# Kernel tuning notes

Measured on AMD Instinct MI355X. Metric: run time of the kernel, lower is better.

## Reference

```python
import jax, jax.numpy as jnp
import numpy as np

BS, S, D, H, KVH, HD = 2, 2048, 2048, 32, 8, 64
N_REP = H // KVH
N_DOCS = 4


def setup_inputs() -> dict:
    key = jax.random.key(0)
    ks = jax.random.split(key, 7)
    x = jax.random.normal(ks[0], (BS, S, D), dtype=jnp.float32)
    # RoPE table (llama theta=10000), stored as real (cos, sin) pairs: [S, HD//2, 2]
    inv_freq = 1.0 / (10000.0 ** (jnp.arange(0, HD, 2, dtype=jnp.float32) / HD))
    ang = jnp.arange(S, dtype=jnp.float32)[:, None] * inv_freq[None, :]  # [S, HD//2]
    freqs_cis = jnp.stack([jnp.cos(ang), jnp.sin(ang)], axis=-1)
    # packed-document ids, non-decreasing along sequence: [BS, S]
    sequence_id = jnp.sort(
        jax.random.randint(ks[1], (BS, S), 0, N_DOCS, dtype=jnp.int32), axis=-1
    )
    std = 0.02
    wq = jax.random.normal(ks[2], (H * HD, D), dtype=jnp.float32) * std
    wk = jax.random.normal(ks[3], (KVH * HD, D), dtype=jnp.float32) * std
    wv = jax.random.normal(ks[4], (KVH * HD, D), dtype=jnp.float32) * std
    wo = jax.random.normal(ks[5], (D, H * HD), dtype=jnp.float32) * std
    return {"x": x, "freqs_cis": freqs_cis, "sequence_id": sequence_id,
            "wq": wq, "wk": wk, "wv": wv, "wo": wo}


def _apply_rope(t, freqs_cis):
    # t: [b, s, h, hd]; freqs_cis: [s, hd//2, 2] (cos, sin)
    b, s, h, hd = t.shape
    tp = t.reshape(b, s, h, hd // 2, 2)
    t0, t1 = tp[..., 0], tp[..., 1]
    cos = freqs_cis[None, :, None, :, 0]
    sin = freqs_cis[None, :, None, :, 1]
    o0 = t0 * cos - t1 * sin
    o1 = t0 * sin + t1 * cos
    return jnp.stack([o0, o1], axis=-1).reshape(b, s, h, hd)


def reference(x, freqs_cis, sequence_id, wq, wk, wv, wo):
    bs, s, _ = x.shape
    xq = (x @ wq.T).reshape(bs, s, H, HD)
    xk = (x @ wk.T).reshape(bs, s, KVH, HD)
    xv = (x @ wv.T).reshape(bs, s, KVH, HD)
    xq = _apply_rope(xq, freqs_cis)
    xk = _apply_rope(xk, freqs_cis)
    # GQA without materializing repeated KV: group queries by kv head
    q = xq.reshape(bs, s, KVH, N_REP, HD).transpose(0, 2, 3, 1, 4)  # [b,g,r,s,d]
    k = xk.transpose(0, 2, 1, 3)  # [b,g,s,d]
    v = xv.transpose(0, 2, 1, 3)  # [b,g,s,d]
    scale = 1.0 / jnp.sqrt(jnp.float32(HD))
    scores = jnp.einsum("bgrqd,bgkd->bgrqk", q, k) * scale
    # document-causal mask: same sequence_id AND causal
    causal = jnp.tril(jnp.ones((s, s), dtype=bool))
    same_doc = sequence_id[:, :, None] == sequence_id[:, None, :]  # [b,s,s]
    mask = (causal[None] & same_doc)[:, None, None, :, :]  # [b,1,1,s,s]
    scores = jnp.where(mask, scores, jnp.float32(-1e30))
    probs = jax.nn.softmax(scores, axis=-1)
    out = jnp.einsum("bgrqk,bgkd->bgrqd", probs, v)  # [b,g,r,s,d]
    out = out.transpose(0, 3, 1, 2, 4).reshape(bs, s, H * HD)
    return out @ wo.T
```

## Files before the change

kernel.cpp:

```cpp
#include <hip/hip_runtime.h>
#include <hip/hip_bf16.h>

typedef __attribute__((ext_vector_type(8))) short bf16x8;
typedef __attribute__((ext_vector_type(4))) float f32x4;

#define MFMA16(A, B, C) __builtin_amdgcn_mfma_f32_16x16x32_bf16(A, B, C, 0, 0, 0)

__device__ __forceinline__ unsigned short f2bf(float f) {
    unsigned int u = __float_as_uint(f);
    u += 0x7fffu + ((u >> 16) & 1u);
    return (unsigned short)(u >> 16);
}
__device__ __forceinline__ float bf2f(unsigned short h) {
    return __uint_as_float(((unsigned int)h) << 16);
}
__device__ __forceinline__ unsigned int pack_bf2(float lo, float hi) {
    __hip_bfloat162 h = __float22bfloat162_rn(make_float2(lo, hi));
    return *reinterpret_cast<unsigned int*>(&h);
}

__device__ __forceinline__ void gload_lds16(const void* g, void* l) {
    __builtin_amdgcn_global_load_lds(
        (__attribute__((address_space(1))) unsigned int*)g,
        (__attribute__((address_space(3))) unsigned int*)l, 16, 0, 0);
}

__device__ __forceinline__ int swz128(int by) {
    return by ^ (((by >> 7) & 7) << 4);
}

__global__ void cvt_kernel(const float* __restrict__ in, unsigned short* __restrict__ out, int n4) {
    const int i = blockIdx.x * 256 + threadIdx.x;
    if (i >= n4) return;
    const float4 v = ((const float4*)in)[i];
    uint2 o;
    o.x = pack_bf2(v.x, v.y);
    o.y = pack_bf2(v.z, v.w);
    ((uint2*)out)[i] = o;
}

__global__ void docstart_kernel(const int* __restrict__ sid, int* __restrict__ ds) {
    const int i = blockIdx.x * 256 + threadIdx.x;
    const int b = i >> 11, s = i & 2047;
    const int* row = sid + b * 2048;
    const int v = row[s];
    int lo = 0, hi = s;
    while (lo < hi) { const int mid = (lo + hi) >> 1; if (row[mid] < v) lo = mid + 1; else hi = mid; }
    ds[i] = lo;
}

#define QKV_K 2048
#define QKV_NT 32
__global__ __launch_bounds__(512, 2) void gemm_qkv8(
    const unsigned short* __restrict__ A,
    const unsigned short* __restrict__ B,
    unsigned short* __restrict__ oq,
    unsigned short* __restrict__ ok,
    unsigned short* __restrict__ ov)
{
    __shared__ __align__(16) unsigned short S[2][2][2][8192];
    const int tid = threadIdx.x, lane = tid & 63, w = tid >> 6;
    const int wr = w >> 2, wc = w & 3;
    const int lr = lane & 15, lc = lane >> 4;

    int bid = blockIdx.x;
    bid = (bid & 7) * 24 + (bid >> 3);
    const int m0 = (bid / 12) * 256, n0 = (bid % 12) * 256;

    const int o0 = (w << 11) + (lane << 4);
    const int o1 = o0 + 1024;
    const int v0 = swz128(o0);
    const int v1 = swz128(o1);
    const int r0 = v0 >> 7, c0 = (v0 & 127) >> 1;
    const int r1 = v1 >> 7, c1 = (v1 & 127) >> 1;
    const size_t aoff0 = (size_t)(m0 + r0) * QKV_K + c0;
    const size_t aoff1 = (size_t)(m0 + r1) * QKV_K + c1;
    const size_t boff0 = (size_t)(n0 + r0) * QKV_K + c0;
    const size_t boff1 = (size_t)(n0 + r1) * QKV_K + c1;
    const int d0 = o0 >> 1, d1 = o1 >> 1;

    f32x4 acc[2][2][4][2];
#pragma unroll
    for (int a = 0; a < 2; a++)
#pragma unroll
        for (int bq = 0; bq < 2; bq++)
#pragma unroll
            for (int i = 0; i < 4; i++)
#pragma unroll
                for (int j = 0; j < 2; j++) acc[a][bq][i][j] = (f32x4){0.f, 0.f, 0.f, 0.f};

    bf16x8 Af[4][2], Bf0[2][2], Bf1[2][2];

    auto STAGE_A = [&](int bf, int h, int kt) {
        gload_lds16(A + aoff0 + (size_t)h * 128 * QKV_K + (size_t)kt * 64, &S[bf][0][h][d0]);
        gload_lds16(A + aoff1 + (size_t)h * 128 * QKV_K + (size_t)kt * 64, &S[bf][0][h][d1]);
    };
    auto STAGE_B = [&](int bf, int h, int kt) {
        gload_lds16(B + boff0 + (size_t)h * 128 * QKV_K + (size_t)kt * 64, &S[bf][1][h][d0]);
        gload_lds16(B + boff1 + (size_t)h * 128 * QKV_K + (size_t)kt * 64, &S[bf][1][h][d1]);
    };
    auto LDA = [&](int bf, int mh) {
#pragma unroll
        for (int i = 0; i < 4; i++)
#pragma unroll
            for (int kh = 0; kh < 2; kh++) {
                const int by = swz128(((wr * 64 + i * 16 + lr) << 7) + (kh << 6) + (lc << 4));
                Af[i][kh] = *(const bf16x8*)((const char*)&S[bf][0][mh][0] + by);
            }
    };
    auto LDB = [&](int bf, int nh, bf16x8 (&Bf)[2][2]) {
#pragma unroll
        for (int j = 0; j < 2; j++)
#pragma unroll
            for (int kh = 0; kh < 2; kh++) {
                const int by = swz128(((wc * 32 + j * 16 + lr) << 7) + (kh << 6) + (lc << 4));
                Bf[j][kh] = *(const bf16x8*)((const char*)&S[bf][1][nh][0] + by);
            }
    };
    auto QUAD = [&](f32x4 (&ac)[4][2], bf16x8 (&Bf)[2][2]) {
        __builtin_amdgcn_s_setprio(1);
#pragma unroll
        for (int i = 0; i < 4; i++)
#pragma unroll
            for (int j = 0; j < 2; j++)
#pragma unroll
                for (int kh = 0; kh < 2; kh++)
                    ac[i][j] = MFMA16(Af[i][kh], Bf[j][kh], ac[i][j]);
        __builtin_amdgcn_s_setprio(0);
    };

#define BAR() __builtin_amdgcn_s_barrier()
#define LGKM0() asm volatile("s_waitcnt lgkmcnt(0)" ::: "memory")

    STAGE_A(0, 0, 0); STAGE_A(0, 1, 0); STAGE_B(0, 0, 0); STAGE_B(0, 1, 0);
    STAGE_A(1, 0, 1); STAGE_B(1, 1, 1); STAGE_A(1, 1, 1);
    asm volatile("s_waitcnt vmcnt(6)" ::: "memory");
    BAR();

    auto GROUP = [&](int g, int bf) {
        LDA(bf, 0); LDB(bf, 0, Bf0);
        if (g + 1 < QKV_NT) STAGE_B(bf ^ 1, 0, g + 1);
        BAR(); LGKM0();
        QUAD(acc[0][0], Bf0);
        BAR();
        LDB(bf, 1, Bf1);
        if (g + 2 < QKV_NT) STAGE_A(bf, 0, g + 2);
        BAR(); LGKM0();
        QUAD(acc[0][1], Bf1);
        BAR();
        LDA(bf, 1);
        if (g + 2 < QKV_NT) STAGE_B(bf, 1, g + 2);
        BAR(); LGKM0();
        QUAD(acc[1][1], Bf1);
        BAR();
        if (g + 2 < QKV_NT) STAGE_A(bf, 1, g + 2);
        BAR();
        QUAD(acc[1][0], Bf0);
        if (g == QKV_NT - 2) { asm volatile("s_waitcnt vmcnt(0)" ::: "memory"); }
        else                 { asm volatile("s_waitcnt vmcnt(6)" ::: "memory"); }
        BAR();
    };

#pragma unroll 1
    for (int g = 0; g < QKV_NT; g += 2) {
        GROUP(g, 0);
        GROUP(g + 1, 1);
    }

#pragma unroll
    for (int mh = 0; mh < 2; mh++)
#pragma unroll
        for (int nh = 0; nh < 2; nh++)
#pragma unroll
            for (int i = 0; i < 4; i++)
#pragma unroll
                for (int j = 0; j < 2; j++) {
                    const int n = n0 + nh * 128 + wc * 32 + j * 16 + lr;
                    const int d = n & 63;
                    const int hh6 = n >> 6;
#pragma unroll
                    for (int r = 0; r < 4; r++) {
                        const int m = m0 + mh * 128 + wr * 64 + i * 16 + lc * 4 + r;
                        const int bb = m >> 11, s = m & 2047;
                        const unsigned short val = f2bf(acc[mh][nh][i][j][r]);
                        if (n < 2048) {
                            oq[((((size_t)bb * 32 + hh6) * 2048 + s) << 6) + d] = val;
                        } else if (n < 2560) {
                            ok[((((size_t)bb * 8 + (hh6 - 32)) * 2048 + s) << 6) + d] = val;
                        } else {
                            ov[((((size_t)bb * 8 + (hh6 - 40)) * 2048 + s) << 6) + d] = val;
                        }
                    }
                }
}
#undef BAR
#undef LGKM0

template <int EPI>
__global__ __launch_bounds__(256) void gemm_bt(
    const unsigned short* __restrict__ A,
    const unsigned short* __restrict__ B,
    int K, int N,
    unsigned short* __restrict__ oq,
    unsigned short* __restrict__ ok,
    unsigned short* __restrict__ ov,
    float* __restrict__ of)
{
    __shared__ __align__(16) unsigned short sA[128 * 32];
    __shared__ __align__(16) unsigned short sB[128 * 32];
    const int tid = threadIdx.x;
    const int lane = tid & 63, wave = tid >> 6;
    const int wr = wave >> 1, wc = wave & 1;
    const int lr = lane & 15, lc = lane >> 4;

    int bid = blockIdx.y * gridDim.x + blockIdx.x;
    const int cpx = (gridDim.x * gridDim.y) >> 3;
    bid = (bid & 7) * cpx + (bid >> 3);
    const int m0 = (bid / gridDim.x) * 128, n0 = (bid % gridDim.x) * 128;

    f32x4 acc[4][4];
#pragma unroll
    for (int i = 0; i < 4; i++)
#pragma unroll
        for (int j = 0; j < 4; j++) acc[i][j] = (f32x4){0.f, 0.f, 0.f, 0.f};

    const int u0 = tid, u1 = tid + 256;
    for (int k0 = 0; k0 < K; k0 += 32) {
        __syncthreads();
        gload_lds16(A + (size_t)(m0 + (u0 >> 2)) * K + k0 + (u0 & 3) * 8, &sA[u0 * 8]);
        gload_lds16(A + (size_t)(m0 + (u1 >> 2)) * K + k0 + (u1 & 3) * 8, &sA[u1 * 8]);
        gload_lds16(B + (size_t)(n0 + (u0 >> 2)) * K + k0 + (u0 & 3) * 8, &sB[u0 * 8]);
        gload_lds16(B + (size_t)(n0 + (u1 >> 2)) * K + k0 + (u1 & 3) * 8, &sB[u1 * 8]);
        __syncthreads();
        bf16x8 af[4], bfv[4];
#pragma unroll
        for (int i = 0; i < 4; i++) {
            af[i]  = *(const bf16x8*)&sA[(wr * 64 + i * 16 + lr) * 32 + lc * 8];
            bfv[i] = *(const bf16x8*)&sB[(wc * 64 + i * 16 + lr) * 32 + lc * 8];
        }
#pragma unroll
        for (int i = 0; i < 4; i++)
#pragma unroll
            for (int j = 0; j < 4; j++) acc[i][j] = MFMA16(af[i], bfv[j], acc[i][j]);
    }

    if (EPI == 0) {
#pragma unroll
        for (int i = 0; i < 4; i++) {
#pragma unroll
            for (int j = 0; j < 4; j++) {
                const int n = n0 + wc * 64 + j * 16 + lr;
                const int d = n & 63;
#pragma unroll
                for (int r = 0; r < 4; r++) {
                    const int m = m0 + wr * 64 + i * 16 + lc * 4 + r;
                    const int bb = m >> 11, s = m & 2047;
                    const unsigned short val = f2bf(acc[i][j][r]);
                    if (n < 2048) {
                        const int hh = n >> 6;
                        oq[((((size_t)bb * 32 + hh) * 2048 + s) << 6) + d] = val;
                    } else if (n < 2560) {
                        const int hh = (n >> 6) - 32;
                        ok[((((size_t)bb * 8 + hh) * 2048 + s) << 6) + d] = val;
                    } else {
                        const int hh = (n >> 6) - 40;
                        ov[((((size_t)bb * 8 + hh) * 2048 + s) << 6) + d] = val;
                    }
                }
            }
        }
    } else {
#pragma unroll
        for (int i = 0; i < 4; i++)
#pragma unroll
            for (int j = 0; j < 4; j++)
#pragma unroll
                for (int r = 0; r < 4; r++) {
                    const int m = m0 + wr * 64 + i * 16 + lc * 4 + r;
                    const int n = n0 + wc * 64 + j * 16 + lr;
                    of[(size_t)m * N + n] = acc[i][j][r];
                }
    }
}

__global__ void rope_kernel(unsigned short* __restrict__ Qb,
                            unsigned short* __restrict__ Kb,
                            const float* __restrict__ fc)
{
    const int NQ = 2 * 32 * 2048 * 32;
    int i = blockIdx.x * 256 + threadIdx.x;
    unsigned short* base;
    if (i < NQ) base = Qb;
    else { base = Kb; i -= NQ; }
    const int p = i & 31, s = (i >> 5) & 2047, bh = i >> 16;
    const size_t off = (((size_t)bh * 2048 + s) << 6) + p * 2;
    const unsigned int w = *(const unsigned int*)&base[off];
    const float t0 = bf2f((unsigned short)(w & 0xffffu));
    const float t1 = bf2f((unsigned short)(w >> 16));
    const float c = fc[(s * 32 + p) * 2], sn = fc[(s * 32 + p) * 2 + 1];
    *(unsigned int*)&base[off] = pack_bf2(t0 * c - t1 * sn, t0 * sn + t1 * c);
}

__global__ __launch_bounds__(256) void attn_kernel(
    const unsigned short* __restrict__ Q,
    const unsigned short* __restrict__ K,
    const unsigned short* __restrict__ V,
    const int* __restrict__ dstart,
    unsigned short* __restrict__ AO)
{
    const int qt = 31 - blockIdx.x;
    const int h = blockIdx.y, b = blockIdx.z;
    const int kvh = h >> 2;
    const int tid = threadIdx.x, lane = tid & 63, wave = tid >> 6;
    const int lr = lane & 15, lc = lane >> 4;
    const int q0 = qt * 64;
    const int qw = q0 + wave * 16;

    __shared__ __align__(16) unsigned short sK[64 * 64];
    __shared__ __align__(16) unsigned short sVt[64][72];

    const unsigned short* Qh = Q + (((size_t)b * 32 + h) * 2048) * 64;
    const unsigned short* Kh = K + (((size_t)b * 8 + kvh) * 2048) * 64;
    const unsigned short* Vh = V + (((size_t)b * 8 + kvh) * 2048) * 64;

    const bf16x8 qf0 = *(const bf16x8*)&Qh[(size_t)(qw + lr) * 64 + lc * 8];
    const bf16x8 qf1 = *(const bf16x8*)&Qh[(size_t)(qw + lr) * 64 + 32 + lc * 8];

    const int qglob = qw + lr;
    const int dsl = dstart[b * 2048 + qglob];
    const int ds_wmin = dstart[b * 2048 + qw];
    const int t0 = dstart[b * 2048 + q0] & ~63;

    float mrow = -1e30f, lrow = 0.f;
    f32x4 oacc[4];
#pragma unroll
    for (int j = 0; j < 4; j++) oacc[j] = (f32x4){0.f, 0.f, 0.f, 0.f};

    for (int t = t0; t < q0 + 64; t += 64) {
        __syncthreads();
        {
            int slot = tid;
            int r = slot >> 3, c = slot & 7;
            gload_lds16(Kh + (size_t)(t + r) * 64 + ((c ^ (r & 7)) * 8), &sK[slot * 8]);
            slot = tid + 256; r = slot >> 3; c = slot & 7;
            gload_lds16(Kh + (size_t)(t + r) * 64 + ((c ^ (r & 7)) * 8), &sK[slot * 8]);
        }
        {
            const int w8 = wave * 8;
            const uint4 va = *(const uint4*)&Vh[(size_t)(t + lane) * 64 + w8];
            const uint4 vb = *(const uint4*)&Vh[(size_t)(t + lane) * 64 + 32 + w8];
            const unsigned short* pa = (const unsigned short*)&va;
            const unsigned short* pb = (const unsigned short*)&vb;
#pragma unroll
            for (int e = 0; e < 8; e++) sVt[w8 + e][lane] = pa[e];
#pragma unroll
            for (int e = 0; e < 8; e++) sVt[32 + w8 + e][lane] = pb[e];
        }
        asm volatile("s_waitcnt vmcnt(0)" ::: "memory");
        __syncthreads();
        if (t > qw + 15 || t + 63 < ds_wmin) continue;

        f32x4 sc[4];
#pragma unroll
        for (int kk = 0; kk < 4; kk++) {
            const int krow = kk * 16 + lr;
            const bf16x8 kf0 = *(const bf16x8*)&sK[krow * 64 + ((lc ^ (lr & 7)) * 8)];
            const bf16x8 kf1 = *(const bf16x8*)&sK[krow * 64 + (((4 + lc) ^ (lr & 7)) * 8)];
            f32x4 a = (f32x4){0.f, 0.f, 0.f, 0.f};
            a = MFMA16(kf0, qf0, a);
            a = MFMA16(kf1, qf1, a);
            sc[kk] = a;
        }
        float vmax = -3e38f;
#pragma unroll
        for (int kk = 0; kk < 4; kk++)
#pragma unroll
            for (int r = 0; r < 4; r++) {
                const int kpos = t + kk * 16 + lc * 4 + r;
                const bool okm = (kpos <= qglob) && (kpos >= dsl);
                sc[kk][r] = okm ? sc[kk][r] * 0.125f : -3e38f;
                vmax = fmaxf(vmax, sc[kk][r]);
            }
        vmax = fmaxf(vmax, __shfl_xor(vmax, 16));
        vmax = fmaxf(vmax, __shfl_xor(vmax, 32));
        const float mnew = fmaxf(mrow, vmax);
        const float corr = __expf(mrow - mnew);
        mrow = mnew;

        float rsum = 0.f;
        unsigned int pk[4][2];
#pragma unroll
        for (int kk = 0; kk < 4; kk++) {
            const float p0 = __expf(sc[kk][0] - mnew);
            const float p1 = __expf(sc[kk][1] - mnew);
            const float p2 = __expf(sc[kk][2] - mnew);
            const float p3 = __expf(sc[kk][3] - mnew);
            rsum += (p0 + p1) + (p2 + p3);
            pk[kk][0] = pack_bf2(p0, p1);
            pk[kk][1] = pack_bf2(p2, p3);
        }
        rsum += __shfl_xor(rsum, 16);
        rsum += __shfl_xor(rsum, 32);
        lrow = lrow * corr + rsum;
#pragma unroll
        for (int j = 0; j < 4; j++)
#pragma unroll
            for (int r = 0; r < 4; r++) oacc[j][r] *= corr;

        const int srcEven = 32 * (lc & 1) + lr;
        const int srcOdd  = srcEven + 16;
        const bool hiKK = (lc & 2) != 0;
        union { unsigned int w[4]; bf16x8 v; } B0, B1;
        {
            unsigned int a, c;
            a = __shfl(pk[0][0], srcEven); c = __shfl(pk[1][0], srcEven); B0.w[0] = hiKK ? c : a;
            a = __shfl(pk[0][1], srcEven); c = __shfl(pk[1][1], srcEven); B0.w[1] = hiKK ? c : a;
            a = __shfl(pk[0][0], srcOdd);  c = __shfl(pk[1][0], srcOdd);  B0.w[2] = hiKK ? c : a;
            a = __shfl(pk[0][1], srcOdd);  c = __shfl(pk[1][1], srcOdd);  B0.w[3] = hiKK ? c : a;
            a = __shfl(pk[2][0], srcEven); c = __shfl(pk[3][0], srcEven); B1.w[0] = hiKK ? c : a;
            a = __shfl(pk[2][1], srcEven); c = __shfl(pk[3][1], srcEven); B1.w[1] = hiKK ? c : a;
            a = __shfl(pk[2][0], srcOdd);  c = __shfl(pk[3][0], srcOdd);  B1.w[2] = hiKK ? c : a;
            a = __shfl(pk[2][1], srcOdd);  c = __shfl(pk[3][1], srcOdd);  B1.w[3] = hiKK ? c : a;
        }

#pragma unroll
        for (int j = 0; j < 4; j++) {
            const bf16x8 a0 = *(const bf16x8*)&sVt[j * 16 + lr][lc * 8];
            const bf16x8 a1 = *(const bf16x8*)&sVt[j * 16 + lr][32 + lc * 8];
            oacc[j] = MFMA16(a0, B0.v, oacc[j]);
            oacc[j] = MFMA16(a1, B1.v, oacc[j]);
        }
    }

    __syncthreads();
    const float inv = 1.0f / lrow;
#pragma unroll
    for (int j = 0; j < 4; j++)
#pragma unroll
        for (int p = 0; p < 2; p++) {
            const unsigned int w = pack_bf2(oacc[j][2 * p] * inv, oacc[j][2 * p + 1] * inv);
            *(unsigned int*)&sVt[wave * 16 + lr][j * 16 + lc * 4 + 2 * p] = w;
        }
    __syncthreads();
#pragma unroll
    for (int half = 0; half < 2; half++) {
        const int c = lane + 64 * half;
        const int row = c >> 3, ch = c & 7;
        const uint4 o = *(const uint4*)&sVt[wave * 16 + row][ch * 8];
        *(uint4*)&AO[((size_t)b * 2048 + qw + row) * 2048 + h * 64 + ch * 8] = o;
    }
}

extern "C" void kernel_launch(void* const* d_in, const int* in_sizes, int n_in,
                              void* d_out, int out_size, void* d_ws, size_t ws_size,
                              hipStream_t stream) {
    const float* x  = (const float*)d_in[0];
    const float* fc = (const float*)d_in[1];
    const int* sid  = (const int*)d_in[2];
    const float* wq = (const float*)d_in[3];
    const float* wk = (const float*)d_in[4];
    const float* wv = (const float*)d_in[5];
    const float* wo = (const float*)d_in[6];
    float* out = (float*)d_out;

    unsigned short* xb   = (unsigned short*)d_ws;
    unsigned short* wqkv = xb + (size_t)4096 * 2048;
    unsigned short* wob  = wqkv + (size_t)3072 * 2048;
    unsigned short* Qb   = wob + (size_t)2048 * 2048;
    unsigned short* Kb   = Qb + (size_t)2 * 32 * 2048 * 64;
    unsigned short* Vb   = Kb + (size_t)2 * 8 * 2048 * 64;
    unsigned short* AO   = Vb + (size_t)2 * 8 * 2048 * 64;
    int* dstart = (int*)(AO + (size_t)4096 * 2048);

    cvt_kernel<<<8192, 256, 0, stream>>>(x, xb, 2097152);
    cvt_kernel<<<4096, 256, 0, stream>>>(wq, wqkv, 1048576);
    cvt_kernel<<<1024, 256, 0, stream>>>(wk, wqkv + (size_t)2048 * 2048, 262144);
    cvt_kernel<<<1024, 256, 0, stream>>>(wv, wqkv + (size_t)2560 * 2048, 262144);
    cvt_kernel<<<4096, 256, 0, stream>>>(wo, wob, 1048576);
    docstart_kernel<<<16, 256, 0, stream>>>(sid, dstart);
    gemm_qkv8<<<dim3(192), 512, 0, stream>>>(xb, wqkv, Qb, Kb, Vb);
    rope_kernel<<<20480, 256, 0, stream>>>(Qb, Kb, fc);
    attn_kernel<<<dim3(32, 32, 2), 256, 0, stream>>>(Qb, Kb, Vb, dstart, AO);
    gemm_bt<1><<<dim3(16, 32), 256, 0, stream>>>(AO, wob, 2048, 2048, nullptr, nullptr, nullptr, out);
}
```

Measured before the change: 209.4 us.

## Fuse RoPE into QKV GEMM epilogue, merge converts, double-buffer attention K/V

Five fp32-to-bf16 conversion launches become one kernel. RoPE moves into the QKV GEMM epilogue: each pair partner comes from a lane shuffle and cos/sin are read from the table, so the separate RoPE read-modify-write pass over Q and K goes away. The attention kernel double-buffers its K/V shared-memory tiles, prefetching the next tile while the current one is computed, at the cost of twice the LDS and possibly lower occupancy.

```diff
diff --git a/kernel.cpp b/kernel.cpp
--- a/kernel.cpp
+++ b/kernel.cpp
@@ -29,14 +29,26 @@
     return by ^ (((by >> 7) & 7) << 4);
 }
 
-__global__ void cvt_kernel(const float* __restrict__ in, unsigned short* __restrict__ out, int n4) {
+__global__ void cvt_all_kernel(const float* __restrict__ x,  const float* __restrict__ wq,
+                               const float* __restrict__ wk, const float* __restrict__ wv,
+                               const float* __restrict__ wo,
+                               unsigned short* __restrict__ xb,
+                               unsigned short* __restrict__ wqkv,
+                               unsigned short* __restrict__ wob) {
     const int i = blockIdx.x * 256 + threadIdx.x;
-    if (i >= n4) return;
-    const float4 v = ((const float4*)in)[i];
+    const float* src;
+    unsigned short* dst;
+    int off;
+    if (i < 2097152)      { src = x;  dst = xb;   off = i; }
+    else if (i < 3145728) { src = wq; dst = wqkv; off = i - 2097152; }
+    else if (i < 3407872) { src = wk; dst = wqkv + (size_t)2048 * 2048; off = i - 3145728; }
+    else if (i < 3670016) { src = wv; dst = wqkv + (size_t)2560 * 2048; off = i - 3407872; }
+    else                  { src = wo; dst = wob;  off = i - 3670016; }
+    const float4 v = ((const float4*)src)[off];
     uint2 o;
     o.x = pack_bf2(v.x, v.y);
     o.y = pack_bf2(v.z, v.w);
-    ((uint2*)out)[i] = o;
+    ((uint2*)dst)[off] = o;
 }
 
 __global__ void docstart_kernel(const int* __restrict__ sid, int* __restrict__ ds) {
@@ -54,6 +66,7 @@
 __global__ __launch_bounds__(512, 2) void gemm_qkv8(
     const unsigned short* __restrict__ A,
     const unsigned short* __restrict__ B,
+    const float* __restrict__ fc,
     unsigned short* __restrict__ oq,
     unsigned short* __restrict__ ok,
     unsigned short* __restrict__ ov)
@@ -69,8 +82,7 @@
 
     const int o0 = (w << 11) + (lane << 4);
     const int o1 = o0 + 1024;
-    const int v0 = swz128(o0);
-    const int v1 = swz128(o1);
+    const int v0 = swz128(o0), v1 = swz128(o1);
     const int r0 = v0 >> 7, c0 = (v0 & 127) >> 1;
     const int r1 = v1 >> 7, c1 = (v1 & 127) >> 1;
     const size_t aoff0 = (size_t)(m0 + r0) * QKV_K + c0;
@@ -177,12 +189,21 @@
                 for (int j = 0; j < 2; j++) {
                     const int n = n0 + nh * 128 + wc * 32 + j * 16 + lr;
                     const int d = n & 63;
+                    const int p = d >> 1;
                     const int hh6 = n >> 6;
+                    const bool isV = (n >= 2560);
 #pragma unroll
                     for (int r = 0; r < 4; r++) {
                         const int m = m0 + mh * 128 + wr * 64 + i * 16 + lc * 4 + r;
                         const int bb = m >> 11, s = m & 2047;
-                        const unsigned short val = f2bf(acc[mh][nh][i][j][r]);
+                        float v = acc[mh][nh][i][j][r];
+                        const float pv = __shfl_xor(v, 1);
+                        if (!isV) {
+                            const float2 cs = *(const float2*)&fc[((s << 5) + p) << 1];
+                            v = (d & 1) ? fmaf(v, cs.x, pv * cs.y)
+                                        : fmaf(v, cs.x, -pv * cs.y);
+                        }
+                        const unsigned short val = f2bf(v);
                         if (n < 2048) {
                             oq[((((size_t)bb * 32 + hh6) * 2048 + s) << 6) + d] = val;
                         } else if (n < 2560) {
@@ -283,24 +304,6 @@
     }
 }
 
-__global__ void rope_kernel(unsigned short* __restrict__ Qb,
-                            unsigned short* __restrict__ Kb,
-                            const float* __restrict__ fc)
-{
-    const int NQ = 2 * 32 * 2048 * 32;
-    int i = blockIdx.x * 256 + threadIdx.x;
-    unsigned short* base;
-    if (i < NQ) base = Qb;
-    else { base = Kb; i -= NQ; }
-    const int p = i & 31, s = (i >> 5) & 2047, bh = i >> 16;
-    const size_t off = (((size_t)bh * 2048 + s) << 6) + p * 2;
-    const unsigned int w = *(const unsigned int*)&base[off];
-    const float t0 = bf2f((unsigned short)(w & 0xffffu));
-    const float t1 = bf2f((unsigned short)(w >> 16));
-    const float c = fc[(s * 32 + p) * 2], sn = fc[(s * 32 + p) * 2 + 1];
-    *(unsigned int*)&base[off] = pack_bf2(t0 * c - t1 * sn, t0 * sn + t1 * c);
-}
-
 __global__ __launch_bounds__(256) void attn_kernel(
     const unsigned short* __restrict__ Q,
     const unsigned short* __restrict__ K,
@@ -316,8 +319,8 @@
     const int q0 = qt * 64;
     const int qw = q0 + wave * 16;
 
-    __shared__ __align__(16) unsigned short sK[64 * 64];
-    __shared__ __align__(16) unsigned short sVt[64][72];
+    __shared__ __align__(16) unsigned short sK[2][64 * 64];
+    __shared__ __align__(16) unsigned short sVt[2][64][72];
 
     const unsigned short* Qh = Q + (((size_t)b * 32 + h) * 2048) * 64;
     const unsigned short* Kh = K + (((size_t)b * 8 + kvh) * 2048) * 64;
@@ -331,87 +334,100 @@
     const int ds_wmin = dstart[b * 2048 + qw];
     const int t0 = dstart[b * 2048 + q0] & ~63;
 
+    const int w8 = wave * 8;
+    const int slot0 = tid,       kr0 = slot0 >> 3, kc0 = slot0 & 7;
+    const int slot1 = tid + 256, kr1 = slot1 >> 3, kc1 = slot1 & 7;
+
+    auto STAGE_K = [&](int t, int c) {
+        gload_lds16(Kh + (size_t)(t + kr0) * 64 + ((kc0 ^ (kr0 & 7)) * 8), &sK[c][slot0 * 8]);
+        gload_lds16(Kh + (size_t)(t + kr1) * 64 + ((kc1 ^ (kr1 & 7)) * 8), &sK[c][slot1 * 8]);
+    };
+    auto WRITE_V = [&](const uint4& va, const uint4& vb, int c) {
+        const unsigned short* pa = (const unsigned short*)&va;
+        const unsigned short* pb = (const unsigned short*)&vb;
+#pragma unroll
+        for (int e = 0; e < 8; e++) sVt[c][w8 + e][lane] = pa[e];
+#pragma unroll
+        for (int e = 0; e < 8; e++) sVt[c][32 + w8 + e][lane] = pb[e];
+    };
+
     float mrow = -1e30f, lrow = 0.f;
     f32x4 oacc[4];
 #pragma unroll
     for (int j = 0; j < 4; j++) oacc[j] = (f32x4){0.f, 0.f, 0.f, 0.f};
 
-    for (int t = t0; t < q0 + 64; t += 64) {
-        __syncthreads();
-        {
-            int slot = tid;
-            int r = slot >> 3, c = slot & 7;
-            gload_lds16(Kh + (size_t)(t + r) * 64 + ((c ^ (r & 7)) * 8), &sK[slot * 8]);
-            slot = tid + 256; r = slot >> 3; c = slot & 7;
-            gload_lds16(Kh + (size_t)(t + r) * 64 + ((c ^ (r & 7)) * 8), &sK[slot * 8]);
-        }
-        {
-            const int w8 = wave * 8;
-            const uint4 va = *(const uint4*)&Vh[(size_t)(t + lane) * 64 + w8];
-            const uint4 vb = *(const uint4*)&Vh[(size_t)(t + lane) * 64 + 32 + w8];
-            const unsigned short* pa = (const unsigned short*)&va;
-            const unsigned short* pb = (const unsigned short*)&vb;
-#pragma unroll
-            for (int e = 0; e < 8; e++) sVt[w8 + e][lane] = pa[e];
-#pragma unroll
-            for (int e = 0; e < 8; e++) sVt[32 + w8 + e][lane] = pb[e];
-        }
+    STAGE_K(t0, 0);
+    {
+        const uint4 va = *(const uint4*)&Vh[(size_t)(t0 + lane) * 64 + w8];
+        const uint4 vb = *(const uint4*)&Vh[(size_t)(t0 + lane) * 64 + 32 + w8];
         asm volatile("s_waitcnt vmcnt(0)" ::: "memory");
-        __syncthreads();
-        if (t > qw + 15 || t + 63 < ds_wmin) continue;
-
-        f32x4 sc[4];
-#pragma unroll
-        for (int kk = 0; kk < 4; kk++) {
-            const int krow = kk * 16 + lr;
-            const bf16x8 kf0 = *(const bf16x8*)&sK[krow * 64 + ((lc ^ (lr & 7)) * 8)];
-            const bf16x8 kf1 = *(const bf16x8*)&sK[krow * 64 + (((4 + lc) ^ (lr & 7)) * 8)];
-            f32x4 a = (f32x4){0.f, 0.f, 0.f, 0.f};
-            a = MFMA16(kf0, qf0, a);
-            a = MFMA16(kf1, qf1, a);
-            sc[kk] = a;
-        }
-        float vmax = -3e38f;
-#pragma unroll
-        for (int kk = 0; kk < 4; kk++)
-#pragma unroll
-            for (int r = 0; r < 4; r++) {
-                const int kpos = t + kk * 16 + lc * 4 + r;
-                const bool okm = (kpos <= qglob) && (kpos >= dsl);
-                sc[kk][r] = okm ? sc[kk][r] * 0.125f : -3e38f;
-                vmax = fmaxf(vmax, sc[kk][r]);
+        WRITE_V(va, vb, 0);
+    }
+    __syncthreads();
+
+    int cb = 0;
+    for (int t = t0; t < q0 + 64; t += 64, cb ^= 1) {
+        const bool more = (t < q0);
+        uint4 va, vb;
+        if (more) {
+            STAGE_K(t + 64, cb ^ 1);
+            va = *(const uint4*)&Vh[(size_t)(t + 64 + lane) * 64 + w8];
+            vb = *(const uint4*)&Vh[(size_t)(t + 64 + lane) * 64 + 32 + w8];
+        }
+        const bool act = !(t > qw + 15 || t + 63 < ds_wmin);
+        union { unsigned int w[4]; bf16x8 v; } B0, B1;
+
+        if (act) {
+            f32x4 sc[4];
+#pragma unroll
+            for (int kk = 0; kk < 4; kk++) {
+                const int krow = kk * 16 + lr;
+                const bf16x8 kf0 = *(const bf16x8*)&sK[cb][krow * 64 + ((lc ^ (lr & 7)) * 8)];
+                const bf16x8 kf1 = *(const bf16x8*)&sK[cb][krow * 64 + (((4 + lc) ^ (lr & 7)) * 8)];
+                f32x4 a = (f32x4){0.f, 0.f, 0.f, 0.f};
+                a = MFMA16(kf0, qf0, a);
+                a = MFMA16(kf1, qf1, a);
+                sc[kk] = a;
             }
-        vmax = fmaxf(vmax, __shfl_xor(vmax, 16));
-        vmax = fmaxf(vmax, __shfl_xor(vmax, 32));
-        const float mnew = fmaxf(mrow, vmax);
-        const float corr = __expf(mrow - mnew);
-        mrow = mnew;
-
-        float rsum = 0.f;
-        unsigned int pk[4][2];
-#pragma unroll
-        for (int kk = 0; kk < 4; kk++) {
-            const float p0 = __expf(sc[kk][0] - mnew);
-            const float p1 = __expf(sc[kk][1] - mnew);
-            const float p2 = __expf(sc[kk][2] - mnew);
-            const float p3 = __expf(sc[kk][3] - mnew);
-            rsum += (p0 + p1) + (p2 + p3);
-            pk[kk][0] = pack_bf2(p0, p1);
-            pk[kk][1] = pack_bf2(p2, p3);
-        }
-        rsum += __shfl_xor(rsum, 16);
-        rsum += __shfl_xor(rsum, 32);
-        lrow = lrow * corr + rsum;
-#pragma unroll
-        for (int j = 0; j < 4; j++)
-#pragma unroll
-            for (int r = 0; r < 4; r++) oacc[j][r] *= corr;
-
-        const int srcEven = 32 * (lc & 1) + lr;
-        const int srcOdd  = srcEven + 16;
-        const bool hiKK = (lc & 2) != 0;
-        union { unsigned int w[4]; bf16x8 v; } B0, B1;
-        {
+            float vmax = -3e38f;
+#pragma unroll
+            for (int kk = 0; kk < 4; kk++)
+#pragma unroll
+                for (int r = 0; r < 4; r++) {
+                    const int kpos = t + kk * 16 + lc * 4 + r;
+                    const bool okm = (kpos <= qglob) && (kpos >= dsl);
+                    sc[kk][r] = okm ? sc[kk][r] * 0.125f : -3e38f;
+                    vmax = fmaxf(vmax, sc[kk][r]);
+                }
+            vmax = fmaxf(vmax, __shfl_xor(vmax, 16));
+            vmax = fmaxf(vmax, __shfl_xor(vmax, 32));
+            const float mnew = fmaxf(mrow, vmax);
+            const float corr = __expf(mrow - mnew);
+            mrow = mnew;
+
+            float rsum = 0.f;
+            unsigned int pk[4][2];
+#pragma unroll
+            for (int kk = 0; kk < 4; kk++) {
+                const float p0 = __expf(sc[kk][0] - mnew);
+                const float p1 = __expf(sc[kk][1] - mnew);
+                const float p2 = __expf(sc[kk][2] - mnew);
+                const float p3 = __expf(sc[kk][3] - mnew);
+                rsum += (p0 + p1) + (p2 + p3);
+                pk[kk][0] = pack_bf2(p0, p1);
+                pk[kk][1] = pack_bf2(p2, p3);
+            }
+            rsum += __shfl_xor(rsum, 16);
+            rsum += __shfl_xor(rsum, 32);
+            lrow = lrow * corr + rsum;
+#pragma unroll
+            for (int j = 0; j < 4; j++)
+#pragma unroll
+                for (int r = 0; r < 4; r++) oacc[j][r] *= corr;
+
+            const int srcEven = 32 * (lc & 1) + lr;
+            const int srcOdd  = srcEven + 16;
+            const bool hiKK = (lc & 2) != 0;
             unsigned int a, c;
             a = __shfl(pk[0][0], srcEven); c = __shfl(pk[1][0], srcEven); B0.w[0] = hiKK ? c : a;
             a = __shfl(pk[0][1], srcEven); c = __shfl(pk[1][1], srcEven); B0.w[1] = hiKK ? c : a;
@@ -423,30 +439,37 @@
             a = __shfl(pk[2][1], srcOdd);  c = __shfl(pk[3][1], srcOdd);  B1.w[3] = hiKK ? c : a;
         }
 
-#pragma unroll
-        for (int j = 0; j < 4; j++) {
-            const bf16x8 a0 = *(const bf16x8*)&sVt[j * 16 + lr][lc * 8];
-            const bf16x8 a1 = *(const bf16x8*)&sVt[j * 16 + lr][32 + lc * 8];
-            oacc[j] = MFMA16(a0, B0.v, oacc[j]);
-            oacc[j] = MFMA16(a1, B1.v, oacc[j]);
-        }
+        if (more) {
+            asm volatile("s_waitcnt vmcnt(0)" ::: "memory");
+            WRITE_V(va, vb, cb ^ 1);
+        }
+
+        if (act) {
+#pragma unroll
+            for (int j = 0; j < 4; j++) {
+                const bf16x8 a0 = *(const bf16x8*)&sVt[cb][j * 16 + lr][lc * 8];
+                const bf16x8 a1 = *(const bf16x8*)&sVt[cb][j * 16 + lr][32 + lc * 8];
+                oacc[j] = MFMA16(a0, B0.v, oacc[j]);
+                oacc[j] = MFMA16(a1, B1.v, oacc[j]);
+            }
+        }
+        __syncthreads();
     }
 
-    __syncthreads();
     const float inv = 1.0f / lrow;
 #pragma unroll
     for (int j = 0; j < 4; j++)
 #pragma unroll
         for (int p = 0; p < 2; p++) {
             const unsigned int w = pack_bf2(oacc[j][2 * p] * inv, oacc[j][2 * p + 1] * inv);
-            *(unsigned int*)&sVt[wave * 16 + lr][j * 16 + lc * 4 + 2 * p] = w;
+            *(unsigned int*)&sVt[0][wave * 16 + lr][j * 16 + lc * 4 + 2 * p] = w;
         }
     __syncthreads();
 #pragma unroll
     for (int half = 0; half < 2; half++) {
         const int c = lane + 64 * half;
         const int row = c >> 3, ch = c & 7;
-        const uint4 o = *(const uint4*)&sVt[wave * 16 + row][ch * 8];
+        const uint4 o = *(const uint4*)&sVt[0][wave * 16 + row][ch * 8];
         *(uint4*)&AO[((size_t)b * 2048 + qw + row) * 2048 + h * 64 + ch * 8] = o;
     }
 }
@@ -472,14 +495,9 @@
     unsigned short* AO   = Vb + (size_t)2 * 8 * 2048 * 64;
     int* dstart = (int*)(AO + (size_t)4096 * 2048);
 
-    cvt_kernel<<<8192, 256, 0, stream>>>(x, xb, 2097152);
-    cvt_kernel<<<4096, 256, 0, stream>>>(wq, wqkv, 1048576);
-    cvt_kernel<<<1024, 256, 0, stream>>>(wk, wqkv + (size_t)2048 * 2048, 262144);
-    cvt_kernel<<<1024, 256, 0, stream>>>(wv, wqkv + (size_t)2560 * 2048, 262144);
-    cvt_kernel<<<4096, 256, 0, stream>>>(wo, wob, 1048576);
+    cvt_all_kernel<<<18432, 256, 0, stream>>>(x, wq, wk, wv, wo, xb, wqkv, wob);
     docstart_kernel<<<16, 256, 0, stream>>>(sid, dstart);
-    gemm_qkv8<<<dim3(192), 512, 0, stream>>>(xb, wqkv, Qb, Kb, Vb);
-    rope_kernel<<<20480, 256, 0, stream>>>(Qb, Kb, fc);
+    gemm_qkv8<<<dim3(192), 512, 0, stream>>>(xb, wqkv, fc, Qb, Kb, Vb);
     attn_kernel<<<dim3(32, 32, 2), 256, 0, stream>>>(Qb, Kb, Vb, dstart, AO);
     gemm_bt<1><<<dim3(16, 32), 256, 0, stream>>>(AO, wob, 2048, 2048, nullptr, nullptr, nullptr, out);
 }
```

New measurement: 216.8 us. 1.04x slower.
